# Kernel optimization log

Hardware: AMD Instinct MI355X
Metric: run time of the kernel (lower is better)

## Reference

```python
import jax, jax.numpy as jnp
import numpy as np

N_HEAD = 16

def setup_inputs() -> dict:
    key = jax.random.key(0)
    kx, kq, kk, kv, kp = jax.random.split(key, 5)
    B, T, C = 4, 2048, 1024
    scale = 1.0 / np.sqrt(C)
    x = jax.random.normal(kx, (B, T, C), dtype=jnp.float32)
    Wq = jax.random.normal(kq, (C, C), dtype=jnp.float32) * scale
    Wk = jax.random.normal(kk, (C, C), dtype=jnp.float32) * scale
    Wv = jax.random.normal(kv, (C, C), dtype=jnp.float32) * scale
    Wp = jax.random.normal(kp, (C, C), dtype=jnp.float32) * scale
    return {"x": x, "Wq": Wq, "Wk": Wk, "Wv": Wv, "Wp": Wp}

def reference(x, Wq, Wk, Wv, Wp):
    B, T, C = x.shape
    H = N_HEAD
    D = C // H
    # projections (nn.Linear, no bias): x @ W^T
    q = (x @ Wq.T).reshape(B, T, H, D).transpose(0, 2, 1, 3)  # [B,H,T,D]
    k = (x @ Wk.T).reshape(B, T, H, D).transpose(0, 2, 1, 3)
    v = (x @ Wv.T).reshape(B, T, H, D).transpose(0, 2, 1, 3)
    att = jnp.einsum('bhqd,bhkd->bhqk', q, k) / jnp.sqrt(jnp.float32(D))
    causal = jnp.tril(jnp.ones((T, T), dtype=bool))
    att = jnp.where(causal, att, -jnp.inf)
    att = jax.nn.softmax(att, axis=-1)
    # dropout p=0.0 -> identity
    y = jnp.einsum('bhqk,bhkd->bhqd', att, v)  # [B,H,T,D]
    y = y.transpose(0, 2, 1, 3).reshape(B, T, C)
    return y @ Wp.T
```

## Files before the change

kernel.cpp:

```cpp
#include <hip/hip_runtime.h>

typedef __bf16 bfrag __attribute__((ext_vector_type(8)));
typedef __bf16 bh4 __attribute__((ext_vector_type(4)));
typedef float f4 __attribute__((ext_vector_type(4)));

#define AS1C(p) (const __attribute__((address_space(1))) void*)(p)
#define AS3(p)  (__attribute__((address_space(3))) void*)(p)

#define QSCALE 0.18033688011112042f

__device__ __forceinline__ void g2l16(const __bf16* g, __bf16* l) {
  __builtin_amdgcn_global_load_lds(AS1C(g), AS3(l), 16, 0, 0);
}


__global__ __launch_bounds__(256) void cvt5(
    const float* __restrict__ s0, const float* __restrict__ s1,
    const float* __restrict__ s2, const float* __restrict__ s3,
    const float* __restrict__ s4,
    __bf16* __restrict__ d0, __bf16* __restrict__ d1, __bf16* __restrict__ d2,
    __bf16* __restrict__ d3, __bf16* __restrict__ d4, long n0, long n1) {
  const float* s; __bf16* d; long n;
  switch (blockIdx.y) {
    case 0: s = s0; d = d0; n = n0; break;
    case 1: s = s1; d = d1; n = n1; break;
    case 2: s = s2; d = d2; n = n1; break;
    case 3: s = s3; d = d3; n = n1; break;
    default: s = s4; d = d4; n = n1; break;
  }
  long i = ((long)blockIdx.x * 256 + threadIdx.x) * 8;
  if (i >= n) return;
  float4 a = *(const float4*)(s + i);
  float4 b = *(const float4*)(s + i + 4);
  bfrag o;
  o[0] = (__bf16)a.x; o[1] = (__bf16)a.y; o[2] = (__bf16)a.z; o[3] = (__bf16)a.w;
  o[4] = (__bf16)b.x; o[5] = (__bf16)b.y; o[6] = (__bf16)b.z; o[7] = (__bf16)b.w;
  *(bfrag*)(d + i) = o;
}

__global__ __launch_bounds__(256) void gemm_qkv(
    const __bf16* __restrict__ A, const __bf16* __restrict__ B,
    __bf16* __restrict__ qb, __bf16* __restrict__ kb, __bf16* __restrict__ vt,
    int M, int K) {
  __shared__ __bf16 sbuf[128 * 130];
  __bf16* As = sbuf;
  __bf16* Bs = sbuf + 4096;
  const int tid = threadIdx.x;
  const int wave = tid >> 6, lane = tid & 63;
  const int lm = lane & 15, quad = lane >> 4;
  const int bm = blockIdx.x * 128, bn = blockIdx.y * 128;
  const int wr = (wave >> 1) * 64, wc = (wave & 1) * 64;
  f4 acc[4][4] = {};
  for (int k0 = 0; k0 < K; k0 += 32) {
#pragma unroll
    for (int i = 0; i < 2; ++i) {
      int s = i * 4 + wave;
      int e = s * 512 + lane * 8;
      int r = e >> 5, c = e & 31;
      g2l16(A + (long)(bm + r) * K + k0 + c, As + e);
      g2l16(B + (long)(bn + r) * K + k0 + c, Bs + e);
    }
    __syncthreads();
    bfrag af[4], bg[4];
#pragma unroll
    for (int mi = 0; mi < 4; ++mi)
      af[mi] = *(const bfrag*)(As + (wr + mi * 16 + lm) * 32 + quad * 8);
#pragma unroll
    for (int ni = 0; ni < 4; ++ni)
      bg[ni] = *(const bfrag*)(Bs + (wc + ni * 16 + lm) * 32 + quad * 8);
#pragma unroll
    for (int mi = 0; mi < 4; ++mi)
#pragma unroll
      for (int ni = 0; ni < 4; ++ni)
        acc[mi][ni] = __builtin_amdgcn_mfma_f32_16x16x32_bf16(af[mi], bg[ni], acc[mi][ni], 0, 0, 0);
    __syncthreads();
  }
  if (bn < 2048) {
    __bf16* dst = (bn < 1024) ? qb : kb;
    const float scl = (bn < 1024) ? QSCALE : 1.0f;
    const int nb = bn & 1023;
#pragma unroll
    for (int mi = 0; mi < 4; ++mi)
#pragma unroll
      for (int ni = 0; ni < 4; ++ni)
#pragma unroll
        for (int r = 0; r < 4; ++r) {
          long row = bm + wr + mi * 16 + quad * 4 + r;
          long col = nb + wc + ni * 16 + lm;
          dst[row * 1024 + col] = (__bf16)(acc[mi][ni][r] * scl);
        }
  } else {
#pragma unroll
    for (int mi = 0; mi < 4; ++mi)
#pragma unroll
      for (int ni = 0; ni < 4; ++ni)
#pragma unroll
        for (int r = 0; r < 4; ++r) {
          int d = wc + ni * 16 + lm;
          int tp = (wr ? 64 : 0) + (quad * 4 + r) * 4 + mi;
          sbuf[d * 130 + tp] = (__bf16)acc[mi][ni][r];
        }
    __syncthreads();
    const int bloc = bm >> 11;
    const int tloc = bm & 2047;
#pragma unroll
    for (int p = 0; p < 8; ++p) {
      int d = (tid >> 4) + p * 16;
      int c = (tid & 15) * 8;
      long dglob = (bn - 2048) + d;
      *(bfrag*)(vt + ((long)bloc * 1024 + dglob) * 2048 + tloc + c) =
          *(const bfrag*)(sbuf + d * 130 + c);
    }
  }
}

template <bool OUT_F32>
__global__ __launch_bounds__(256) void gemm_bt_bf16(
    const __bf16* __restrict__ A, const __bf16* __restrict__ B,
    void* __restrict__ Cp, int M, int N, int K) {
  __shared__ __bf16 As[128 * 32];
  __shared__ __bf16 Bs[128 * 32];
  const int tid = threadIdx.x;
  const int wave = tid >> 6, lane = tid & 63;
  const int lm = lane & 15, quad = lane >> 4;
  const int bm = blockIdx.x * 128, bn = blockIdx.y * 128;
  const int wr = (wave >> 1) * 64, wc = (wave & 1) * 64;
  f4 acc[4][4] = {};
  for (int k0 = 0; k0 < K; k0 += 32) {
#pragma unroll
    for (int i = 0; i < 2; ++i) {
      int s = i * 4 + wave;
      int e = s * 512 + lane * 8;
      int r = e >> 5, c = e & 31;
      g2l16(A + (long)(bm + r) * K + k0 + c, As + e);
      g2l16(B + (long)(bn + r) * K + k0 + c, Bs + e);
    }
    __syncthreads();
    bfrag af[4], bg[4];
#pragma unroll
    for (int mi = 0; mi < 4; ++mi)
      af[mi] = *(const bfrag*)(As + (wr + mi * 16 + lm) * 32 + quad * 8);
#pragma unroll
    for (int ni = 0; ni < 4; ++ni)
      bg[ni] = *(const bfrag*)(Bs + (wc + ni * 16 + lm) * 32 + quad * 8);
#pragma unroll
    for (int mi = 0; mi < 4; ++mi)
#pragma unroll
      for (int ni = 0; ni < 4; ++ni)
        acc[mi][ni] = __builtin_amdgcn_mfma_f32_16x16x32_bf16(af[mi], bg[ni], acc[mi][ni], 0, 0, 0);
    __syncthreads();
  }
#pragma unroll
  for (int mi = 0; mi < 4; ++mi)
#pragma unroll
    for (int ni = 0; ni < 4; ++ni)
#pragma unroll
      for (int r = 0; r < 4; ++r) {
        long row = bm + wr + mi * 16 + quad * 4 + r;
        long col = bn + wc + ni * 16 + lm;
        if (OUT_F32) ((float*)Cp)[row * N + col] = acc[mi][ni][r];
        else ((__bf16*)Cp)[row * N + col] = (__bf16)acc[mi][ni][r];
      }
}

template <bool A_F32, bool OUT_F32>
__global__ __launch_bounds__(256) void gemm_bt_cv(
    const void* __restrict__ Ap, const float* __restrict__ Bp,
    void* __restrict__ Cp, int M, int N, int K, float scl) {
  __shared__ __bf16 As[128 * 32];
  __shared__ __bf16 Bs[128 * 32];
  const int tid = threadIdx.x;
  const int lane = tid & 63, wave = tid >> 6;
  const int lm = lane & 15, quad = lane >> 4;
  const int bm = blockIdx.x * 128, bn = blockIdx.y * 128;
  const int wr = (wave >> 1) * 64, wc = (wave & 1) * 64;
  const int e0 = tid * 16, sr = e0 >> 5, sc = e0 & 31;
  f4 acc[4][4] = {};
  for (int k0 = 0; k0 < K; k0 += 32) {
    if (A_F32) {
      const float4* ga = (const float4*)((const float*)Ap + (long)(bm + sr) * K + k0 + sc);
#pragma unroll
      for (int j = 0; j < 4; ++j) {
        float4 v = ga[j];
        As[sr * 32 + sc + j * 4 + 0] = (__bf16)v.x;
        As[sr * 32 + sc + j * 4 + 1] = (__bf16)v.y;
        As[sr * 32 + sc + j * 4 + 2] = (__bf16)v.z;
        As[sr * 32 + sc + j * 4 + 3] = (__bf16)v.w;
      }
    } else {
      const __bf16* Ab = (const __bf16*)Ap + (long)(bm + sr) * K + k0 + sc;
      *(bfrag*)(As + sr * 32 + sc) = *(const bfrag*)Ab;
      *(bfrag*)(As + sr * 32 + sc + 8) = *(const bfrag*)(Ab + 8);
    }
    {
      const float4* gb = (const float4*)(Bp + (long)(bn + sr) * K + k0 + sc);
#pragma unroll
      for (int j = 0; j < 4; ++j) {
        float4 v = gb[j];
        Bs[sr * 32 + sc + j * 4 + 0] = (__bf16)v.x;
        Bs[sr * 32 + sc + j * 4 + 1] = (__bf16)v.y;
        Bs[sr * 32 + sc + j * 4 + 2] = (__bf16)v.z;
        Bs[sr * 32 + sc + j * 4 + 3] = (__bf16)v.w;
      }
    }
    __syncthreads();
    bfrag af[4], bg[4];
#pragma unroll
    for (int mi = 0; mi < 4; ++mi)
      af[mi] = *(const bfrag*)(As + (wr + mi * 16 + lm) * 32 + quad * 8);
#pragma unroll
    for (int ni = 0; ni < 4; ++ni)
      bg[ni] = *(const bfrag*)(Bs + (wc + ni * 16 + lm) * 32 + quad * 8);
#pragma unroll
    for (int mi = 0; mi < 4; ++mi)
#pragma unroll
      for (int ni = 0; ni < 4; ++ni)
        acc[mi][ni] = __builtin_amdgcn_mfma_f32_16x16x32_bf16(af[mi], bg[ni], acc[mi][ni], 0, 0, 0);
    __syncthreads();
  }
#pragma unroll
  for (int mi = 0; mi < 4; ++mi)
#pragma unroll
    for (int ni = 0; ni < 4; ++ni)
#pragma unroll
      for (int r = 0; r < 4; ++r) {
        long row = bm + wr + mi * 16 + quad * 4 + r;
        long col = bn + wc + ni * 16 + lm;
        if (OUT_F32) ((float*)Cp)[row * N + col] = acc[mi][ni][r] * scl;
        else ((__bf16*)Cp)[row * N + col] = (__bf16)(acc[mi][ni][r] * scl);
      }
}

#define KP 72

template <bool DIAG>
__device__ __forceinline__ void attn_tile(
    const bfrag* qf, int row0, int kBase,
    const bfrag* kf, const bfrag* vf, __bf16* Psw,
    int lm, int quad, f4* yacc, f4& Lacc, bfrag ones) {
  f4 sac[4];
#pragma unroll
  for (int sub = 0; sub < 4; ++sub) {
    f4 z = {};
#pragma unroll
    for (int f = 0; f < 2; ++f)
      z = __builtin_amdgcn_mfma_f32_16x16x32_bf16(qf[f], kf[sub * 2 + f], z, 0, 0, 0);
    sac[sub] = z;
  }
#pragma unroll
  for (int r = 0; r < 4; ++r) {
    bh4 pk;
#pragma unroll
    for (int sub = 0; sub < 4; ++sub) {
      float pv = __builtin_amdgcn_exp2f(sac[sub][r]);
      if (DIAG) {
        bool masked = (kBase + sub * 16 + lm > row0 + quad * 4 + r);
        pv = masked ? 0.f : pv;
      }
      pk[sub] = (__bf16)pv;
    }
    *(bh4*)(Psw + (quad * 4 + r) * KP + lm * 4) = pk;
  }
  __asm__ volatile("s_waitcnt lgkmcnt(0)" ::: "memory");
#pragma unroll
  for (int f = 0; f < 2; ++f) {
    bfrag pf = *(const bfrag*)(Psw + lm * KP + f * 32 + quad * 8);
    Lacc = __builtin_amdgcn_mfma_f32_16x16x32_bf16(pf, ones, Lacc, 0, 0, 0);
#pragma unroll
    for (int ds = 0; ds < 4; ++ds)
      yacc[ds] = __builtin_amdgcn_mfma_f32_16x16x32_bf16(pf, vf[ds * 2 + f], yacc[ds], 0, 0, 0);
  }
}

template <bool VT>
__global__ __launch_bounds__(256) void attn_fwd5(
    const __bf16* Qg, const __bf16* __restrict__ Kg,
    const __bf16* __restrict__ Vsrc, __bf16* Yg) {
  const int TT = 2048, CC = 1024;
  __shared__ __bf16 Ks[64 * KP];
  __shared__ __bf16 Vs[64 * KP];
  __shared__ __bf16 Ps[4 * 16 * KP];
  const int tid = threadIdx.x;
  const int wave = tid >> 6, lane = tid & 63;
  const int lm = lane & 15, quad = lane >> 4;
  const int i = blockIdx.x;
  const int qtA = i, qtB = 31 - i;
  const int b = blockIdx.y >> 4, h = blockIdx.y & 15;
  const long rbase = (long)b * TT;
  const int hoff = h * 64;
  const int rowA0 = qtA * 64 + wave * 16, rowB0 = qtB * 64 + wave * 16;
  bfrag qfA[2], qfB[2];
#pragma unroll
  for (int f = 0; f < 2; ++f) {
    qfA[f] = *(const bfrag*)(Qg + (rbase + rowA0 + lm) * CC + hoff + f * 32 + quad * 8);
    qfB[f] = *(const bfrag*)(Qg + (rbase + rowB0 + lm) * CC + hoff + f * 32 + quad * 8);
  }
  bfrag ones;
#pragma unroll
  for (int j = 0; j < 8; ++j) ones[j] = (__bf16)1.0f;
  f4 yA[4] = {}, yB[4] = {};
  f4 LA = {}, LB = {};
  __bf16* Psw = Ps + wave * 16 * KP;
  for (int kt = 0; kt <= qtB; ++kt) {
    const int kBase = kt * 64;
    __syncthreads();
#pragma unroll
    for (int s = 0; s < 2; ++s) {
      int idx = tid + s * 256;
      int r = idx >> 3, c = (idx & 7) * 8;
      *(bfrag*)(Ks + r * KP + c) =
          *(const bfrag*)(Kg + (rbase + kBase + r) * CC + hoff + c);
    }
    if (VT) {
#pragma unroll
      for (int s = 0; s < 2; ++s) {
        int idx = tid + s * 256;
        int d = idx >> 3, kc = (idx & 7) * 8;
        *(bfrag*)(Vs + d * KP + kc) =
            *(const bfrag*)(Vsrc + ((long)b * 1024 + hoff + d) * 2048 + kBase + kc);
      }
    } else {
#pragma unroll
      for (int s = 0; s < 2; ++s) {
        int idx = tid + s * 256;
        int r = idx >> 3, c = (idx & 7) * 8;
        int kp = (r & 15) * 4 + (r >> 4);
        bfrag vv = *(const bfrag*)(Vsrc + (rbase + kBase + r) * CC + hoff + c);
#pragma unroll
        for (int j = 0; j < 8; ++j) Vs[(c + j) * KP + kp] = vv[j];
      }
    }
    __syncthreads();
    bfrag kf[8], vf[8];
#pragma unroll
    for (int sub = 0; sub < 4; ++sub)
#pragma unroll
      for (int f = 0; f < 2; ++f) {
        kf[sub * 2 + f] = *(const bfrag*)(Ks + (sub * 16 + lm) * KP + f * 32 + quad * 8);
        vf[sub * 2 + f] = *(const bfrag*)(Vs + (sub * 16 + lm) * KP + f * 32 + quad * 8);
      }
    if (kt == qtB)
      attn_tile<true>(qfB, rowB0, kBase, kf, vf, Psw, lm, quad, yB, LB, ones);
    else
      attn_tile<false>(qfB, rowB0, kBase, kf, vf, Psw, lm, quad, yB, LB, ones);
    if (kt < qtA)
      attn_tile<false>(qfA, rowA0, kBase, kf, vf, Psw, lm, quad, yA, LA, ones);
    else if (kt == qtA)
      attn_tile<true>(qfA, rowA0, kBase, kf, vf, Psw, lm, quad, yA, LA, ones);
  }
#pragma unroll
  for (int ds = 0; ds < 4; ++ds)
#pragma unroll
    for (int r = 0; r < 4; ++r) {
      long rowa = rbase + rowA0 + quad * 4 + r;
      long rowb = rbase + rowB0 + quad * 4 + r;
      Yg[rowa * CC + hoff + ds * 16 + lm] = (__bf16)(yA[ds][r] / LA[r]);
      Yg[rowb * CC + hoff + ds * 16 + lm] = (__bf16)(yB[ds][r] / LB[r]);
    }
}

extern "C" void kernel_launch(void* const* d_in, const int* in_sizes, int n_in,
                              void* d_out, int out_size, void* d_ws, size_t ws_size,
                              hipStream_t stream) {
  (void)in_sizes; (void)n_in; (void)out_size;
  const float* x  = (const float*)d_in[0];
  const float* Wq = (const float*)d_in[1];
  const float* Wk = (const float*)d_in[2];
  const float* Wv = (const float*)d_in[3];
  const float* Wp = (const float*)d_in[4];
  float* out = (float*)d_out;
  const long R = 8192;
  const long BUF = R * 1024;
  const long WN = 1024L * 1024;
  __bf16* qb = (__bf16*)d_ws;
  __bf16* kb = (__bf16*)d_out;
  __bf16* vslot = kb + BUF;
  dim3 blk(256, 1, 1);
  const size_t need = (size_t)(2 * BUF + 4 * WN) * 2;
  if (ws_size >= need) {
    __bf16* xb = qb + BUF;
    __bf16* wqkv = xb + BUF;
    __bf16* wpb = wqkv + 3 * WN;
    cvt5<<<dim3((unsigned)(BUF / (256 * 8)), 5, 1), blk, 0, stream>>>(
        x, Wq, Wk, Wv, Wp, xb, wqkv, wqkv + WN, wqkv + 2 * WN, wpb, BUF, WN);
    gemm_qkv<<<dim3(64, 24, 1), blk, 0, stream>>>(xb, wqkv, qb, kb, vslot, 8192, 1024);
    attn_fwd5<true><<<dim3(16, 64, 1), blk, 0, stream>>>(qb, kb, vslot, qb);
    gemm_bt_bf16<true><<<dim3(64, 8, 1), blk, 0, stream>>>(qb, wpb, out, 8192, 1024, 1024);
  } else {
    gemm_bt_cv<true, false><<<dim3(64, 8, 1), blk, 0, stream>>>(x, Wq, qb, 8192, 1024, 1024, QSCALE);
    gemm_bt_cv<true, false><<<dim3(64, 8, 1), blk, 0, stream>>>(x, Wk, kb, 8192, 1024, 1024, 1.0f);
    gemm_bt_cv<true, false><<<dim3(64, 8, 1), blk, 0, stream>>>(x, Wv, vslot, 8192, 1024, 1024, 1.0f);
    attn_fwd5<false><<<dim3(16, 64, 1), blk, 0, stream>>>(qb, kb, vslot, qb);
    gemm_bt_cv<false, true><<<dim3(64, 8, 1), blk, 0, stream>>>(qb, Wp, out, 8192, 1024, 1024, 1.0f);
  }
}
```

Baseline: 277.9 us.

## Process four query tiles per attention block and use K=64 GEMM steps

After: 291.3 us. 4.8% more time.

```diff
diff --git a/kernel.cpp b/kernel.cpp
--- a/kernel.cpp
+++ b/kernel.cpp
@@ -12,7 +12,6 @@
 __device__ __forceinline__ void g2l16(const __bf16* g, __bf16* l) {
   __builtin_amdgcn_global_load_lds(AS1C(g), AS3(l), 16, 0, 0);
 }
-
 
 __global__ __launch_bounds__(256) void cvt5(
     const float* __restrict__ s0, const float* __restrict__ s1,
@@ -42,37 +41,48 @@
     const __bf16* __restrict__ A, const __bf16* __restrict__ B,
     __bf16* __restrict__ qb, __bf16* __restrict__ kb, __bf16* __restrict__ vt,
     int M, int K) {
-  __shared__ __bf16 sbuf[128 * 130];
-  __bf16* As = sbuf;
-  __bf16* Bs = sbuf + 4096;
+  __shared__ __bf16 sbuf[16640];
+  __bf16* As0 = sbuf;
+  __bf16* As1 = sbuf + 4096;
+  __bf16* Bs0 = sbuf + 8192;
+  __bf16* Bs1 = sbuf + 12288;
   const int tid = threadIdx.x;
   const int wave = tid >> 6, lane = tid & 63;
   const int lm = lane & 15, quad = lane >> 4;
   const int bm = blockIdx.x * 128, bn = blockIdx.y * 128;
   const int wr = (wave >> 1) * 64, wc = (wave & 1) * 64;
   f4 acc[4][4] = {};
-  for (int k0 = 0; k0 < K; k0 += 32) {
-#pragma unroll
-    for (int i = 0; i < 2; ++i) {
-      int s = i * 4 + wave;
+  for (int k0 = 0; k0 < K; k0 += 64) {
+#pragma unroll
+    for (int ii = 0; ii < 2; ++ii) {
+      int s = ii * 4 + wave;
       int e = s * 512 + lane * 8;
       int r = e >> 5, c = e & 31;
-      g2l16(A + (long)(bm + r) * K + k0 + c, As + e);
-      g2l16(B + (long)(bn + r) * K + k0 + c, Bs + e);
-    }
-    __syncthreads();
-    bfrag af[4], bg[4];
-#pragma unroll
-    for (int mi = 0; mi < 4; ++mi)
-      af[mi] = *(const bfrag*)(As + (wr + mi * 16 + lm) * 32 + quad * 8);
-#pragma unroll
-    for (int ni = 0; ni < 4; ++ni)
-      bg[ni] = *(const bfrag*)(Bs + (wc + ni * 16 + lm) * 32 + quad * 8);
-#pragma unroll
-    for (int mi = 0; mi < 4; ++mi)
+      const __bf16* ar = A + (long)(bm + r) * K + k0 + c;
+      const __bf16* br = B + (long)(bn + r) * K + k0 + c;
+      g2l16(ar, As0 + e);
+      g2l16(ar + 32, As1 + e);
+      g2l16(br, Bs0 + e);
+      g2l16(br + 32, Bs1 + e);
+    }
+    __syncthreads();
+#pragma unroll
+    for (int st = 0; st < 2; ++st) {
+      const __bf16* As = st ? As1 : As0;
+      const __bf16* Bs = st ? Bs1 : Bs0;
+      bfrag af[4], bg[4];
+#pragma unroll
+      for (int mi = 0; mi < 4; ++mi)
+        af[mi] = *(const bfrag*)(As + (wr + mi * 16 + lm) * 32 + quad * 8);
 #pragma unroll
       for (int ni = 0; ni < 4; ++ni)
-        acc[mi][ni] = __builtin_amdgcn_mfma_f32_16x16x32_bf16(af[mi], bg[ni], acc[mi][ni], 0, 0, 0);
+        bg[ni] = *(const bfrag*)(Bs + (wc + ni * 16 + lm) * 32 + quad * 8);
+#pragma unroll
+      for (int mi = 0; mi < 4; ++mi)
+#pragma unroll
+        for (int ni = 0; ni < 4; ++ni)
+          acc[mi][ni] = __builtin_amdgcn_mfma_f32_16x16x32_bf16(af[mi], bg[ni], acc[mi][ni], 0, 0, 0);
+    }
     __syncthreads();
   }
   if (bn < 2048) {
@@ -118,36 +128,48 @@
 __global__ __launch_bounds__(256) void gemm_bt_bf16(
     const __bf16* __restrict__ A, const __bf16* __restrict__ B,
     void* __restrict__ Cp, int M, int N, int K) {
-  __shared__ __bf16 As[128 * 32];
-  __shared__ __bf16 Bs[128 * 32];
+  __shared__ __bf16 sbuf[16384];
+  __bf16* As0 = sbuf;
+  __bf16* As1 = sbuf + 4096;
+  __bf16* Bs0 = sbuf + 8192;
+  __bf16* Bs1 = sbuf + 12288;
   const int tid = threadIdx.x;
   const int wave = tid >> 6, lane = tid & 63;
   const int lm = lane & 15, quad = lane >> 4;
   const int bm = blockIdx.x * 128, bn = blockIdx.y * 128;
   const int wr = (wave >> 1) * 64, wc = (wave & 1) * 64;
   f4 acc[4][4] = {};
-  for (int k0 = 0; k0 < K; k0 += 32) {
-#pragma unroll
-    for (int i = 0; i < 2; ++i) {
-      int s = i * 4 + wave;
+  for (int k0 = 0; k0 < K; k0 += 64) {
+#pragma unroll
+    for (int ii = 0; ii < 2; ++ii) {
+      int s = ii * 4 + wave;
       int e = s * 512 + lane * 8;
       int r = e >> 5, c = e & 31;
-      g2l16(A + (long)(bm + r) * K + k0 + c, As + e);
-      g2l16(B + (long)(bn + r) * K + k0 + c, Bs + e);
-    }
-    __syncthreads();
-    bfrag af[4], bg[4];
-#pragma unroll
-    for (int mi = 0; mi < 4; ++mi)
-      af[mi] = *(const bfrag*)(As + (wr + mi * 16 + lm) * 32 + quad * 8);
-#pragma unroll
-    for (int ni = 0; ni < 4; ++ni)
-      bg[ni] = *(const bfrag*)(Bs + (wc + ni * 16 + lm) * 32 + quad * 8);
-#pragma unroll
-    for (int mi = 0; mi < 4; ++mi)
+      const __bf16* ar = A + (long)(bm + r) * K + k0 + c;
+      const __bf16* br = B + (long)(bn + r) * K + k0 + c;
+      g2l16(ar, As0 + e);
+      g2l16(ar + 32, As1 + e);
+      g2l16(br, Bs0 + e);
+      g2l16(br + 32, Bs1 + e);
+    }
+    __syncthreads();
+#pragma unroll
+    for (int st = 0; st < 2; ++st) {
+      const __bf16* As = st ? As1 : As0;
+      const __bf16* Bs = st ? Bs1 : Bs0;
+      bfrag af[4], bg[4];
+#pragma unroll
+      for (int mi = 0; mi < 4; ++mi)
+        af[mi] = *(const bfrag*)(As + (wr + mi * 16 + lm) * 32 + quad * 8);
 #pragma unroll
       for (int ni = 0; ni < 4; ++ni)
-        acc[mi][ni] = __builtin_amdgcn_mfma_f32_16x16x32_bf16(af[mi], bg[ni], acc[mi][ni], 0, 0, 0);
+        bg[ni] = *(const bfrag*)(Bs + (wc + ni * 16 + lm) * 32 + quad * 8);
+#pragma unroll
+      for (int mi = 0; mi < 4; ++mi)
+#pragma unroll
+        for (int ni = 0; ni < 4; ++ni)
+          acc[mi][ni] = __builtin_amdgcn_mfma_f32_16x16x32_bf16(af[mi], bg[ni], acc[mi][ni], 0, 0, 0);
+    }
     __syncthreads();
   }
 #pragma unroll
@@ -273,7 +295,7 @@
 }
 
 template <bool VT>
-__global__ __launch_bounds__(256) void attn_fwd5(
+__global__ __launch_bounds__(256, 2) void attn_fwd6(
     const __bf16* Qg, const __bf16* __restrict__ Kg,
     const __bf16* __restrict__ Vsrc, __bf16* Yg) {
   const int TT = 2048, CC = 1024;
@@ -284,24 +306,27 @@
   const int wave = tid >> 6, lane = tid & 63;
   const int lm = lane & 15, quad = lane >> 4;
   const int i = blockIdx.x;
-  const int qtA = i, qtB = 31 - i;
+  const int qtv[4] = {i, 15 - i, 16 + i, 31 - i};
   const int b = blockIdx.y >> 4, h = blockIdx.y & 15;
   const long rbase = (long)b * TT;
   const int hoff = h * 64;
-  const int rowA0 = qtA * 64 + wave * 16, rowB0 = qtB * 64 + wave * 16;
-  bfrag qfA[2], qfB[2];
-#pragma unroll
-  for (int f = 0; f < 2; ++f) {
-    qfA[f] = *(const bfrag*)(Qg + (rbase + rowA0 + lm) * CC + hoff + f * 32 + quad * 8);
-    qfB[f] = *(const bfrag*)(Qg + (rbase + rowB0 + lm) * CC + hoff + f * 32 + quad * 8);
+  int row0[4];
+  bfrag qf[4][2];
+#pragma unroll
+  for (int t = 0; t < 4; ++t) {
+    row0[t] = qtv[t] * 64 + wave * 16;
+#pragma unroll
+    for (int f = 0; f < 2; ++f)
+      qf[t][f] = *(const bfrag*)(Qg + (rbase + row0[t] + lm) * CC + hoff + f * 32 + quad * 8);
   }
   bfrag ones;
 #pragma unroll
   for (int j = 0; j < 8; ++j) ones[j] = (__bf16)1.0f;
-  f4 yA[4] = {}, yB[4] = {};
-  f4 LA = {}, LB = {};
+  f4 y[4][4] = {};
+  f4 L[4] = {};
   __bf16* Psw = Ps + wave * 16 * KP;
-  for (int kt = 0; kt <= qtB; ++kt) {
+  const int ktMax = qtv[3];
+  for (int kt = 0; kt <= ktMax; ++kt) {
     const int kBase = kt * 64;
     __syncthreads();
 #pragma unroll
@@ -339,24 +364,23 @@
         kf[sub * 2 + f] = *(const bfrag*)(Ks + (sub * 16 + lm) * KP + f * 32 + quad * 8);
         vf[sub * 2 + f] = *(const bfrag*)(Vs + (sub * 16 + lm) * KP + f * 32 + quad * 8);
       }
-    if (kt == qtB)
-      attn_tile<true>(qfB, rowB0, kBase, kf, vf, Psw, lm, quad, yB, LB, ones);
-    else
-      attn_tile<false>(qfB, rowB0, kBase, kf, vf, Psw, lm, quad, yB, LB, ones);
-    if (kt < qtA)
-      attn_tile<false>(qfA, rowA0, kBase, kf, vf, Psw, lm, quad, yA, LA, ones);
-    else if (kt == qtA)
-      attn_tile<true>(qfA, rowA0, kBase, kf, vf, Psw, lm, quad, yA, LA, ones);
-  }
-#pragma unroll
-  for (int ds = 0; ds < 4; ++ds)
-#pragma unroll
-    for (int r = 0; r < 4; ++r) {
-      long rowa = rbase + rowA0 + quad * 4 + r;
-      long rowb = rbase + rowB0 + quad * 4 + r;
-      Yg[rowa * CC + hoff + ds * 16 + lm] = (__bf16)(yA[ds][r] / LA[r]);
-      Yg[rowb * CC + hoff + ds * 16 + lm] = (__bf16)(yB[ds][r] / LB[r]);
-    }
+#pragma unroll
+    for (int t = 3; t >= 0; --t) {
+      if (kt < qtv[t])
+        attn_tile<false>(qf[t], row0[t], kBase, kf, vf, Psw, lm, quad, y[t], L[t], ones);
+      else if (kt == qtv[t])
+        attn_tile<true>(qf[t], row0[t], kBase, kf, vf, Psw, lm, quad, y[t], L[t], ones);
+    }
+  }
+#pragma unroll
+  for (int t = 0; t < 4; ++t)
+#pragma unroll
+    for (int ds = 0; ds < 4; ++ds)
+#pragma unroll
+      for (int r = 0; r < 4; ++r) {
+        long row = rbase + row0[t] + quad * 4 + r;
+        Yg[row * CC + hoff + ds * 16 + lm] = (__bf16)(y[t][ds][r] / L[t][r]);
+      }
 }
 
 extern "C" void kernel_launch(void* const* d_in, const int* in_sizes, int n_in,
@@ -384,13 +408,13 @@
     cvt5<<<dim3((unsigned)(BUF / (256 * 8)), 5, 1), blk, 0, stream>>>(
         x, Wq, Wk, Wv, Wp, xb, wqkv, wqkv + WN, wqkv + 2 * WN, wpb, BUF, WN);
     gemm_qkv<<<dim3(64, 24, 1), blk, 0, stream>>>(xb, wqkv, qb, kb, vslot, 8192, 1024);
-    attn_fwd5<true><<<dim3(16, 64, 1), blk, 0, stream>>>(qb, kb, vslot, qb);
+    attn_fwd6<true><<<dim3(8, 64, 1), blk, 0, stream>>>(qb, kb, vslot, qb);
     gemm_bt_bf16<true><<<dim3(64, 8, 1), blk, 0, stream>>>(qb, wpb, out, 8192, 1024, 1024);
   } else {
     gemm_bt_cv<true, false><<<dim3(64, 8, 1), blk, 0, stream>>>(x, Wq, qb, 8192, 1024, 1024, QSCALE);
     gemm_bt_cv<true, false><<<dim3(64, 8, 1), blk, 0, stream>>>(x, Wk, kb, 8192, 1024, 1024, 1.0f);
     gemm_bt_cv<true, false><<<dim3(64, 8, 1), blk, 0, stream>>>(x, Wv, vslot, 8192, 1024, 1024, 1.0f);
-    attn_fwd5<false><<<dim3(16, 64, 1), blk, 0, stream>>>(qb, kb, vslot, qb);
+    attn_fwd6<false><<<dim3(8, 64, 1), blk, 0, stream>>>(qb, kb, vslot, qb);
     gemm_bt_cv<false, true><<<dim3(64, 8, 1), blk, 0, stream>>>(qb, Wp, out, 8192, 1024, 1024, 1.0f);
   }
 }
```
